# Performance work log

Hardware: AMD Instinct MI355X
Metric: run time of the kernel (lower is better)

## Reference

```python
import jax, jax.numpy as jnp
import numpy as np

HEAD_SIZE = 64
N_EMBD = 1024
B, T = 8, 4096

def setup_inputs() -> dict:
    key = jax.random.key(0)
    k1, k2, k3, k4 = jax.random.split(key, 4)
    x = jax.random.normal(k1, (B, T, N_EMBD), dtype=jnp.float32)
    # bias-free Linear weights, stored as [in, out] so y = x @ W
    scale = 1.0 / np.sqrt(N_EMBD)
    Wk = jax.random.uniform(k2, (N_EMBD, HEAD_SIZE), jnp.float32, -scale, scale)
    Wq = jax.random.uniform(k3, (N_EMBD, HEAD_SIZE), jnp.float32, -scale, scale)
    Wv = jax.random.uniform(k4, (N_EMBD, HEAD_SIZE), jnp.float32, -scale, scale)
    return {"x": x, "Wk": Wk, "Wq": Wq, "Wv": Wv}

def reference(x, Wk, Wq, Wv):
    # x: [B, T, C]
    k = x @ Wk  # [B, T, H]
    q = x @ Wq
    v = x @ Wv
    scale = HEAD_SIZE ** -0.5
    wei = jnp.einsum('bth,bsh->bts', q, k) * scale  # [B, T, T]
    Tn = x.shape[1]
    causal = jnp.tril(jnp.ones((Tn, Tn), dtype=bool))
    wei = jnp.where(causal, wei, -jnp.inf)
    wei = jax.nn.softmax(wei, axis=-1)
    # dropout p=0.0 -> identity (eval behavior)
    out = jnp.einsum('bts,bsh->bth', wei, v)  # [B, T, H]
    return out
```

## Files before the change

kernel.cpp:

```cpp
#include <hip/hip_runtime.h>
#include <hip/hip_bf16.h>


#define HS 64
#define NE 1024
#define NB 8
#define TS 4096
#define NROW (NB * TS)

#define QKV_BUF 20480
#define QKV_XB  12288

typedef __attribute__((ext_vector_type(4)))  float f32x4;
typedef __attribute__((ext_vector_type(16))) float f32x16;
typedef __attribute__((ext_vector_type(8)))  short s16x8;
typedef __attribute__((ext_vector_type(4)))  float vfloat4;

__device__ __forceinline__ unsigned short f2bf(float x) {
  return __builtin_bit_cast(unsigned short, __float2bfloat16(x));
}
__device__ __forceinline__ unsigned pkbf(float lo, float hi) {
  return (unsigned)f2bf(lo) | ((unsigned)f2bf(hi) << 16);
}

union ABFrag { s16x8 v; unsigned d[4]; };

__device__ __forceinline__ void gl_lds16(const void* g, const unsigned char* l) {
  __builtin_amdgcn_global_load_lds(
      (const __attribute__((address_space(1))) unsigned int*)(g),
      (__attribute__((address_space(3))) unsigned int*)(l), 16, 0, 0);
}

__global__ __launch_bounds__(256) void wt_kernel(const float* __restrict__ Wk,
                                                 const float* __restrict__ Wq,
                                                 const float* __restrict__ Wv,
                                                 unsigned short* __restrict__ wT2) {
  int gid = blockIdx.x * 256 + threadIdx.x;
  int j = gid & 7;
  int t1 = gid >> 3;
  int sk = t1 % 768;
  int c  = t1 / 768;
  int g = sk / 192, n = sk % 192;
  int k = c * 32 + g * 8 + j;
  const float* W = (n < 64) ? Wq : (n < 128) ? Wk : Wv;
  float s = (n < 64) ? 0.18033688011112042f : 1.0f;
  wT2[gid] = f2bf(W[k * 64 + (n & 63)] * s);
}

__global__ __launch_bounds__(256, 4) void qkv_kernel(const float* __restrict__ x,
                                                     const unsigned short* __restrict__ wT2,
                                                     unsigned short* __restrict__ q_ws,
                                                     unsigned short* __restrict__ kf,
                                                     unsigned short* __restrict__ vf) {
  __shared__ __align__(16) unsigned char smem[2 * QKV_BUF];
  const int t = threadIdx.x;
  const int w = t >> 6, lane = t & 63;
  const int g = lane >> 4, nn = lane & 15;
  const int m0blk = blockIdx.x * 64;
  const int m0 = m0blk + w * 16;

  f32x4 acc[12];
#pragma unroll
  for (int i = 0; i < 12; ++i) acc[i] = f32x4{0.f, 0.f, 0.f, 0.f};

  const unsigned short* wsrcA = wT2 + (size_t)(w * 192 + lane) * 8;
  const int wd0 = w * 3072;
  const float* xs0 = x + (size_t)(m0blk + w * 16 + 0 + (lane >> 3)) * NE + (lane & 7) * 4;
  const float* xs1 = x + (size_t)(m0blk + w * 16 + 8 + (lane >> 3)) * NE + (lane & 7) * 4;
  const int xd0 = QKV_XB + w * 2048;
  const int xd1 = xd0 + 1024;

  const int abase = QKV_XB + (w * 16 + nn) * 128 + g * 32;
  const int wbase = (g * 192 + nn) * 16;

#define ISSUE(C)                                                               \
  {                                                                            \
    unsigned char* db_ = smem + ((C) & 1) * QKV_BUF;                           \
    gl_lds16(wsrcA + (size_t)(C) * 6144, db_ + wd0);                           \
    gl_lds16(wsrcA + (size_t)(C) * 6144 + 512, db_ + wd0 + 1024);              \
    gl_lds16(wsrcA + (size_t)(C) * 6144 + 1024, db_ + wd0 + 2048);             \
    gl_lds16(xs0 + (C) * 32, db_ + xd0);                                       \
    gl_lds16(xs1 + (C) * 32, db_ + xd1);                                       \
  }

  ISSUE(0)
  __builtin_amdgcn_sched_barrier(0);
  ISSUE(1)
  __builtin_amdgcn_sched_barrier(0);

#define PHASE(C, VM, DOISS)                                                    \
  {                                                                            \
    asm volatile("s_waitcnt vmcnt(" #VM ")" ::: "memory");                     \
    __builtin_amdgcn_s_barrier();                                              \
    __builtin_amdgcn_sched_barrier(0);                                         \
    const unsigned char* bb_ = smem + ((C) & 1) * QKV_BUF;                     \
    const vfloat4 a0_ = *(const vfloat4*)(bb_ + abase);                        \
    const vfloat4 a1_ = *(const vfloat4*)(bb_ + abase + 16);                   \
    ABFrag af;                                                                 \
    af.d[0] = pkbf(a0_.x, a0_.y); af.d[1] = pkbf(a0_.z, a0_.w);                \
    af.d[2] = pkbf(a1_.x, a1_.y); af.d[3] = pkbf(a1_.z, a1_.w);                \
    _Pragma("unroll")                                                          \
    for (int i = 0; i < 12; ++i) {                                             \
      const s16x8 bf = *(const s16x8*)(bb_ + wbase + i * 256);                 \
      acc[i] = __builtin_amdgcn_mfma_f32_16x16x32_bf16(af.v, bf, acc[i], 0, 0, 0); \
    }                                                                          \
    __builtin_amdgcn_sched_barrier(0);                                         \
    __builtin_amdgcn_s_barrier();                                              \
    __builtin_amdgcn_sched_barrier(0);                                         \
    if (DOISS) { ISSUE((C) + 2) }                                              \
    __builtin_amdgcn_sched_barrier(0);                                         \
  }

#pragma unroll
  for (int c = 0; c < 30; ++c) PHASE(c, 5, 1)
  PHASE(30, 5, 0)
  PHASE(31, 0, 0)
#undef PHASE
#undef ISSUE

  const int rbase = m0 + 4 * g;
#pragma unroll
  for (int i = 0; i < 12; ++i) {
    const int c = 16 * i + nn;
#pragma unroll
    for (int j = 0; j < 4; ++j) {
      const int rr = rbase + j;
      const unsigned short hval = f2bf(acc[i][j]);
      const int b = rr >> 12, tt = rr & 4095;
      if (c < 64) {
        q_ws[(size_t)rr * HS + c] = hval;
      } else if (c < 128) {
        const int h = c - 64;
        const size_t idx = (size_t)b * 262144 + (size_t)(tt >> 5) * 2048 +
                           (h >> 4) * 512 + ((h >> 3) & 1) * 256 +
                           (tt & 31) * 8 + (h & 7);
        kf[idx] = hval;
      } else {
        const int h = c - 128;
        const size_t idx = (size_t)b * 262144 + (size_t)(tt >> 5) * 2048 +
                           (h >> 5) * 1024 + ((tt >> 4) & 1) * 512 +
                           ((tt >> 3) & 1) * 256 + (h & 31) * 8 + (tt & 7);
        vf[idx] = hval;
      }
    }
  }
}

#define TILE32F(DIAG, KF, VF, QF, M_RUN, L_RUN, O)                             \
  {                                                                            \
    f32x16 st_;                                                                \
    _Pragma("unroll") for (int r = 0; r < 16; ++r) st_[r] = 0.f;               \
    __builtin_amdgcn_s_setprio(1);                                             \
    st_ = __builtin_amdgcn_mfma_f32_32x32x16_bf16(KF[0], QF[0], st_, 0, 0, 0); \
    st_ = __builtin_amdgcn_mfma_f32_32x32x16_bf16(KF[1], QF[1], st_, 0, 0, 0); \
    st_ = __builtin_amdgcn_mfma_f32_32x32x16_bf16(KF[2], QF[2], st_, 0, 0, 0); \
    st_ = __builtin_amdgcn_mfma_f32_32x32x16_bf16(KF[3], QF[3], st_, 0, 0, 0); \
    __builtin_amdgcn_s_setprio(0);                                             \
    if (DIAG) {                                                                \
      _Pragma("unroll") for (int r = 0; r < 16; ++r) {                         \
        const int kvl_ = (r & 3) + 8 * (r >> 2) + hi4;                         \
        if (kvl_ > qi) st_[r] = -1e30f;                                        \
      }                                                                        \
    }                                                                          \
    float mx_ =                                                                \
      fmaxf(fmaxf(fmaxf(fmaxf(st_[0], st_[1]), fmaxf(st_[2], st_[3])),         \
                  fmaxf(fmaxf(st_[4], st_[5]), fmaxf(st_[6], st_[7]))),        \
            fmaxf(fmaxf(fmaxf(st_[8], st_[9]), fmaxf(st_[10], st_[11])),       \
                  fmaxf(fmaxf(st_[12], st_[13]), fmaxf(st_[14], st_[15]))));   \
    mx_ = fmaxf(mx_, __shfl_xor(mx_, 32, 64));                                 \
    const float mn_ = fmaxf(M_RUN, mx_);                                       \
    if (__ballot(mn_ > M_RUN)) {                                               \
      const float fs_ = __builtin_amdgcn_exp2f(M_RUN - mn_);                   \
      _Pragma("unroll") for (int r = 0; r < 16; ++r) {                         \
        O[0][r] *= fs_; O[1][r] *= fs_;                                        \
      }                                                                        \
      L_RUN *= fs_;                                                            \
      M_RUN = mn_;                                                             \
    }                                                                          \
    float p_[16];                                                              \
    _Pragma("unroll") for (int r = 0; r < 16; ++r)                             \
      p_[r] = __builtin_amdgcn_exp2f(st_[r] - M_RUN);                          \
    float sm_ = ((p_[0] + p_[1]) + (p_[2] + p_[3])) +                          \
                ((p_[4] + p_[5]) + (p_[6] + p_[7]));                           \
    sm_ += ((p_[8] + p_[9]) + (p_[10] + p_[11])) +                             \
           ((p_[12] + p_[13]) + (p_[14] + p_[15]));                            \
    sm_ += __shfl_xor(sm_, 32, 64);                                            \
    L_RUN += sm_;                                                              \
    const unsigned q01_ = pkbf(p_[0], p_[1]),   q23_ = pkbf(p_[2], p_[3]);     \
    const unsigned q45_ = pkbf(p_[4], p_[5]),   q67_ = pkbf(p_[6], p_[7]);     \
    const unsigned q89_ = pkbf(p_[8], p_[9]),   qab_ = pkbf(p_[10], p_[11]);   \
    const unsigned qcd_ = pkbf(p_[12], p_[13]), qef_ = pkbf(p_[14], p_[15]);   \
    const unsigned t01_ = (unsigned)__shfl_xor((int)q01_, 32, 64);             \
    const unsigned t23_ = (unsigned)__shfl_xor((int)q23_, 32, 64);             \
    const unsigned t45_ = (unsigned)__shfl_xor((int)q45_, 32, 64);             \
    const unsigned t67_ = (unsigned)__shfl_xor((int)q67_, 32, 64);             \
    const unsigned t89_ = (unsigned)__shfl_xor((int)q89_, 32, 64);             \
    const unsigned tab_ = (unsigned)__shfl_xor((int)qab_, 32, 64);             \
    const unsigned tcd_ = (unsigned)__shfl_xor((int)qcd_, 32, 64);             \
    const unsigned tef_ = (unsigned)__shfl_xor((int)qef_, 32, 64);             \
    ABFrag pf0_, pf1_;                                                         \
    pf0_.d[0] = hi ? t45_ : q01_;                                              \
    pf0_.d[1] = hi ? t67_ : q23_;                                              \
    pf0_.d[2] = hi ? q45_ : t01_;                                              \
    pf0_.d[3] = hi ? q67_ : t23_;                                              \
    pf1_.d[0] = hi ? tcd_ : q89_;                                              \
    pf1_.d[1] = hi ? tef_ : qab_;                                              \
    pf1_.d[2] = hi ? qcd_ : t89_;                                              \
    pf1_.d[3] = hi ? qef_ : tab_;                                              \
    __builtin_amdgcn_s_setprio(1);                                             \
    O[0] = __builtin_amdgcn_mfma_f32_32x32x16_bf16(VF[0], pf0_.v, O[0], 0,0,0);\
    O[0] = __builtin_amdgcn_mfma_f32_32x32x16_bf16(VF[1], pf1_.v, O[0], 0,0,0);\
    O[1] = __builtin_amdgcn_mfma_f32_32x32x16_bf16(VF[2], pf0_.v, O[1], 0,0,0);\
    O[1] = __builtin_amdgcn_mfma_f32_32x32x16_bf16(VF[3], pf1_.v, O[1], 0,0,0);\
    __builtin_amdgcn_s_setprio(0);                                             \
  }

#define LD4(dst, base)                                                         \
  dst[0] = *(const s16x8*)(base);                                              \
  dst[1] = *(const s16x8*)((base) + 512);                                      \
  dst[2] = *(const s16x8*)((base) + 1024);                                     \
  dst[3] = *(const s16x8*)((base) + 1536);

__global__ __launch_bounds__(256, 2) void attn_kernel(const unsigned short* __restrict__ q_ws,
                                                      const unsigned short* __restrict__ kf,
                                                      const unsigned short* __restrict__ vf,
                                                      float* __restrict__ out) {
  __shared__ float o_sm[2][4][16][68];
  __shared__ float lm_sm[2][4][32][2];

  const int wv = threadIdx.x >> 6, lane = threadIdx.x & 63;
  const int qi = lane & 31, hi = lane >> 5;
  const int hi8 = 8 * hi, hi4 = 4 * hi;

  const int bid = blockIdx.x;
  const int b = bid & 7;
  const int pr = bid >> 3;
  const int tiA = pr, tiB = 127 - pr;
  const int t0A = tiA * 32, t0B = tiB * 32;

  const unsigned short* kfb = kf + (size_t)b * 262144 + lane * 8;
  const unsigned short* vfb = vf + (size_t)b * 262144 + lane * 8;
  const unsigned short* qrA = q_ws + (size_t)(b * TS + t0A + qi) * HS + hi8;
  const unsigned short* qrB = q_ws + (size_t)(b * TS + t0B + qi) * HS + hi8;

  s16x8 qfA[4], qfB[4];
#pragma unroll
  for (int kk = 0; kk < 4; ++kk) {
    qfA[kk] = *(const s16x8*)(qrA + 16 * kk);
    qfB[kk] = *(const s16x8*)(qrB + 16 * kk);
  }

  f32x16 oA[2], oB[2];
#pragma unroll
  for (int r = 0; r < 16; ++r) { oA[0][r] = 0.f; oA[1][r] = 0.f; oB[0][r] = 0.f; oB[1][r] = 0.f; }
  float mA = -1e30f, lA = 0.f, mB = -1e30f, lB = 0.f;

  const int ntA = tiA + 1, ntB = tiB + 1;

  s16x8 kA[4], kB[4];
  LD4(kA, kfb + (size_t)((wv < ntA) ? wv : 0) * 2048)
  LD4(kB, kfb + (size_t)wv * 2048)

  for (int it = wv; it < ntB; it += 4) {
    const bool dA = it < ntA;
    const int nxt = it + 4;
    s16x8 vA[4], vB[4];
    LD4(vA, vfb + (size_t)(dA ? it : 0) * 2048)
    LD4(vB, vfb + (size_t)it * 2048)
    s16x8 kAn[4], kBn[4];
    LD4(kAn, kfb + (size_t)((nxt < ntA) ? nxt : 0) * 2048)
    LD4(kBn, kfb + (size_t)((nxt < ntB) ? nxt : 0) * 2048)

    if (dA) TILE32F(it == tiA, kA, vA, qfA, mA, lA, oA)
    TILE32F(it == tiB, kB, vB, qfB, mB, lB, oB)

#pragma unroll
    for (int kk = 0; kk < 4; ++kk) { kA[kk] = kAn[kk]; kB[kk] = kBn[kk]; }
  }

  if (lane < 32) {
    lm_sm[0][wv][lane][0] = mA; lm_sm[0][wv][lane][1] = lA;
    lm_sm[1][wv][lane][0] = mB; lm_sm[1][wv][lane][1] = lB;
  }
  const int q8 = (threadIdx.x >> 3) & 15;
  const int h0 = (threadIdx.x & 7) * 8;
  const int X  = threadIdx.x >> 7;
  const int t0X = X ? t0B : t0A;

#pragma unroll
  for (int P = 0; P < 2; ++P) {
    if ((qi >> 4) == P) {
      const int qr = qi & 15;
#pragma unroll
      for (int ht = 0; ht < 2; ++ht)
#pragma unroll
        for (int r = 0; r < 16; ++r) {
          const int h = ht * 32 + (r & 3) + 8 * (r >> 2) + hi4;
          o_sm[0][wv][qr][h] = oA[ht][r];
          o_sm[1][wv][qr][h] = oB[ht][r];
        }
    }
    __syncthreads();
    {
      const int q = 16 * P + q8;
      const float m0v = lm_sm[X][0][q][0], m1v = lm_sm[X][1][q][0];
      const float m2v = lm_sm[X][2][q][0], m3v = lm_sm[X][3][q][0];
      const float M = fmaxf(fmaxf(m0v, m1v), fmaxf(m2v, m3v));
      const float w0 = __builtin_amdgcn_exp2f(m0v - M);
      const float w1 = __builtin_amdgcn_exp2f(m1v - M);
      const float w2 = __builtin_amdgcn_exp2f(m2v - M);
      const float w3 = __builtin_amdgcn_exp2f(m3v - M);
      const float L = w0 * lm_sm[X][0][q][1] + w1 * lm_sm[X][1][q][1] +
                      w2 * lm_sm[X][2][q][1] + w3 * lm_sm[X][3][q][1];
      const float inv = 1.0f / L;
      float rv[8];
#pragma unroll
      for (int j = 0; j < 8; ++j)
        rv[j] = (w0 * o_sm[X][0][q8][h0 + j] + w1 * o_sm[X][1][q8][h0 + j] +
                 w2 * o_sm[X][2][q8][h0 + j] + w3 * o_sm[X][3][q8][h0 + j]) * inv;
      float* ob = out + ((size_t)(b * TS + t0X + q)) * HS + h0;
      *(float4*)(ob)     = float4{rv[0], rv[1], rv[2], rv[3]};
      *(float4*)(ob + 4) = float4{rv[4], rv[5], rv[6], rv[7]};
    }
    if (P == 0) __syncthreads();
  }
}

extern "C" void kernel_launch(void* const* d_in, const int* in_sizes, int n_in,
                              void* d_out, int out_size, void* d_ws, size_t ws_size,
                              hipStream_t stream) {
  const float* x  = (const float*)d_in[0];
  const float* Wk = (const float*)d_in[1];
  const float* Wq = (const float*)d_in[2];
  const float* Wv = (const float*)d_in[3];
  float* out = (float*)d_out;

  unsigned short* wT2  = (unsigned short*)d_ws;
  unsigned short* q_ws = wT2 + 192 * 1024;
  unsigned short* kf   = q_ws + (size_t)NROW * HS;
  unsigned short* vf   = kf + (size_t)NROW * HS;

  wt_kernel<<<dim3(768), dim3(256), 0, stream>>>(Wk, Wq, Wv, wT2);
  qkv_kernel<<<dim3(NROW / 64), dim3(256), 0, stream>>>(x, wT2, q_ws, kf, vf);
  attn_kernel<<<dim3(512), dim3(256), 0, stream>>>(q_ws, kf, vf, out);
}
```

Measured before the change: 70.98 us.

## Pair batches per block at the same query tile and drop K prefetch

Each block previously handled two mirrored query tiles (ti and 127-ti) of one batch, which gave every block equal work. It now handles the same query tile for two batches (b and b+4), scheduled from the longest causal tile down. The loop is simpler: the per-iteration branch on whether tile A is active is gone and both tiles share the diagonal test. The register double-buffering of K for the next iteration is also removed, so K and V loads are no longer overlapped with compute. Blocks now carry unequal work, which can leave the heaviest blocks setting the tail, and load latency is exposed in exchange for lower register pressure.

```diff
diff --git a/kernel.cpp b/kernel.cpp
--- a/kernel.cpp
+++ b/kernel.cpp
@@ -233,15 +233,17 @@
   const int hi8 = 8 * hi, hi4 = 4 * hi;
 
   const int bid = blockIdx.x;
-  const int b = bid & 7;
-  const int pr = bid >> 3;
-  const int tiA = pr, tiB = 127 - pr;
-  const int t0A = tiA * 32, t0B = tiB * 32;
-
-  const unsigned short* kfb = kf + (size_t)b * 262144 + lane * 8;
-  const unsigned short* vfb = vf + (size_t)b * 262144 + lane * 8;
-  const unsigned short* qrA = q_ws + (size_t)(b * TS + t0A + qi) * HS + hi8;
-  const unsigned short* qrB = q_ws + (size_t)(b * TS + t0B + qi) * HS + hi8;
+  const int ti = 127 - (bid >> 2);
+  const int bA = bid & 3, bB = bA + 4;
+  const int t0 = ti * 32;
+  const int nt = ti + 1;
+
+  const unsigned short* kfA = kf + (size_t)bA * 262144 + lane * 8;
+  const unsigned short* vfA = vf + (size_t)bA * 262144 + lane * 8;
+  const unsigned short* kfB = kf + (size_t)bB * 262144 + lane * 8;
+  const unsigned short* vfB = vf + (size_t)bB * 262144 + lane * 8;
+  const unsigned short* qrA = q_ws + (size_t)(bA * TS + t0 + qi) * HS + hi8;
+  const unsigned short* qrB = q_ws + (size_t)(bB * TS + t0 + qi) * HS + hi8;
 
   s16x8 qfA[4], qfB[4];
 #pragma unroll
@@ -255,27 +257,15 @@
   for (int r = 0; r < 16; ++r) { oA[0][r] = 0.f; oA[1][r] = 0.f; oB[0][r] = 0.f; oB[1][r] = 0.f; }
   float mA = -1e30f, lA = 0.f, mB = -1e30f, lB = 0.f;
 
-  const int ntA = tiA + 1, ntB = tiB + 1;
-
-  s16x8 kA[4], kB[4];
-  LD4(kA, kfb + (size_t)((wv < ntA) ? wv : 0) * 2048)
-  LD4(kB, kfb + (size_t)wv * 2048)
-
-  for (int it = wv; it < ntB; it += 4) {
-    const bool dA = it < ntA;
-    const int nxt = it + 4;
-    s16x8 vA[4], vB[4];
-    LD4(vA, vfb + (size_t)(dA ? it : 0) * 2048)
-    LD4(vB, vfb + (size_t)it * 2048)
-    s16x8 kAn[4], kBn[4];
-    LD4(kAn, kfb + (size_t)((nxt < ntA) ? nxt : 0) * 2048)
-    LD4(kBn, kfb + (size_t)((nxt < ntB) ? nxt : 0) * 2048)
-
-    if (dA) TILE32F(it == tiA, kA, vA, qfA, mA, lA, oA)
-    TILE32F(it == tiB, kB, vB, qfB, mB, lB, oB)
-
-#pragma unroll
-    for (int kk = 0; kk < 4; ++kk) { kA[kk] = kAn[kk]; kB[kk] = kBn[kk]; }
+  for (int it = wv; it < nt; it += 4) {
+    const bool dg = (it == ti);
+    s16x8 kA[4], kB[4], vA[4], vB[4];
+    LD4(kA, kfA + (size_t)it * 2048)
+    LD4(kB, kfB + (size_t)it * 2048)
+    LD4(vA, vfA + (size_t)it * 2048)
+    LD4(vB, vfB + (size_t)it * 2048)
+    TILE32F(dg, kA, vA, qfA, mA, lA, oA)
+    TILE32F(dg, kB, vB, qfB, mB, lB, oB)
   }
 
   if (lane < 32) {
@@ -285,7 +275,7 @@
   const int q8 = (threadIdx.x >> 3) & 15;
   const int h0 = (threadIdx.x & 7) * 8;
   const int X  = threadIdx.x >> 7;
-  const int t0X = X ? t0B : t0A;
+  const int bX = X ? bB : bA;
 
 #pragma unroll
   for (int P = 0; P < 2; ++P) {
@@ -318,7 +308,7 @@
       for (int j = 0; j < 8; ++j)
         rv[j] = (w0 * o_sm[X][0][q8][h0 + j] + w1 * o_sm[X][1][q8][h0 + j] +
                  w2 * o_sm[X][2][q8][h0 + j] + w3 * o_sm[X][3][q8][h0 + j]) * inv;
-      float* ob = out + ((size_t)(b * TS + t0X + q)) * HS + h0;
+      float* ob = out + ((size_t)(bX * TS + t0 + q)) * HS + h0;
       *(float4*)(ob)     = float4{rv[0], rv[1], rv[2], rv[3]};
       *(float4*)(ob + 4) = float4{rv[4], rv[5], rv[6], rv[7]};
     }
```

Result: slower. 78.63 us (+10.8%).

## Split paired query tiles across separate waves with 512-thread attention blocks

Applied to the files above, without the earlier changes.

Each block used 4 waves, and every wave handled both the light and the heavy causal tile. Now it launches 8 waves: waves 0-3 take one tile and waves 4-7 take the paired tile. This halves per-wave register state (one Q/O set instead of two) and lets occupancy rise to 4 blocks of 512 threads. The explicit software prefetch of the next K tile is dropped, and the waves on the light tile finish early and sit idle, so load balance inside a block gets worse.

```diff
diff --git a/kernel.cpp b/kernel.cpp
--- a/kernel.cpp
+++ b/kernel.cpp
@@ -221,7 +221,7 @@
   dst[2] = *(const s16x8*)((base) + 1024);                                     \
   dst[3] = *(const s16x8*)((base) + 1536);
 
-__global__ __launch_bounds__(256, 2) void attn_kernel(const unsigned short* __restrict__ q_ws,
+__global__ __launch_bounds__(512, 4) void attn_kernel(const unsigned short* __restrict__ q_ws,
                                                       const unsigned short* __restrict__ kf,
                                                       const unsigned short* __restrict__ vf,
                                                       float* __restrict__ out) {
@@ -235,74 +235,57 @@
   const int bid = blockIdx.x;
   const int b = bid & 7;
   const int pr = bid >> 3;
-  const int tiA = pr, tiB = 127 - pr;
-  const int t0A = tiA * 32, t0B = tiB * 32;
+  const int tile = wv >> 2;
+  const int wq = wv & 3;
+  const int ti_x = tile ? (127 - pr) : pr;
+  const int t0 = ti_x * 32;
+  const int nt = ti_x + 1;
 
   const unsigned short* kfb = kf + (size_t)b * 262144 + lane * 8;
   const unsigned short* vfb = vf + (size_t)b * 262144 + lane * 8;
-  const unsigned short* qrA = q_ws + (size_t)(b * TS + t0A + qi) * HS + hi8;
-  const unsigned short* qrB = q_ws + (size_t)(b * TS + t0B + qi) * HS + hi8;
-
-  s16x8 qfA[4], qfB[4];
-#pragma unroll
-  for (int kk = 0; kk < 4; ++kk) {
-    qfA[kk] = *(const s16x8*)(qrA + 16 * kk);
-    qfB[kk] = *(const s16x8*)(qrB + 16 * kk);
-  }
-
-  f32x16 oA[2], oB[2];
-#pragma unroll
-  for (int r = 0; r < 16; ++r) { oA[0][r] = 0.f; oA[1][r] = 0.f; oB[0][r] = 0.f; oB[1][r] = 0.f; }
-  float mA = -1e30f, lA = 0.f, mB = -1e30f, lB = 0.f;
-
-  const int ntA = tiA + 1, ntB = tiB + 1;
-
-  s16x8 kA[4], kB[4];
-  LD4(kA, kfb + (size_t)((wv < ntA) ? wv : 0) * 2048)
-  LD4(kB, kfb + (size_t)wv * 2048)
-
-  for (int it = wv; it < ntB; it += 4) {
-    const bool dA = it < ntA;
-    const int nxt = it + 4;
-    s16x8 vA[4], vB[4];
-    LD4(vA, vfb + (size_t)(dA ? it : 0) * 2048)
-    LD4(vB, vfb + (size_t)it * 2048)
-    s16x8 kAn[4], kBn[4];
-    LD4(kAn, kfb + (size_t)((nxt < ntA) ? nxt : 0) * 2048)
-    LD4(kBn, kfb + (size_t)((nxt < ntB) ? nxt : 0) * 2048)
-
-    if (dA) TILE32F(it == tiA, kA, vA, qfA, mA, lA, oA)
-    TILE32F(it == tiB, kB, vB, qfB, mB, lB, oB)
-
-#pragma unroll
-    for (int kk = 0; kk < 4; ++kk) { kA[kk] = kAn[kk]; kB[kk] = kBn[kk]; }
+  const unsigned short* qr = q_ws + (size_t)(b * TS + t0 + qi) * HS + hi8;
+
+  s16x8 qf[4];
+#pragma unroll
+  for (int kk = 0; kk < 4; ++kk) qf[kk] = *(const s16x8*)(qr + 16 * kk);
+
+  f32x16 o[2];
+#pragma unroll
+  for (int r = 0; r < 16; ++r) { o[0][r] = 0.f; o[1][r] = 0.f; }
+  float m_run = -1e30f, l_run = 0.f;
+
+  for (int it = wq; it < nt; it += 4) {
+    s16x8 kfr[4], vfr[4];
+    LD4(kfr, kfb + (size_t)it * 2048)
+    LD4(vfr, vfb + (size_t)it * 2048)
+    TILE32F(it == ti_x, kfr, vfr, qf, m_run, l_run, o)
   }
 
   if (lane < 32) {
-    lm_sm[0][wv][lane][0] = mA; lm_sm[0][wv][lane][1] = lA;
-    lm_sm[1][wv][lane][0] = mB; lm_sm[1][wv][lane][1] = lB;
-  }
-  const int q8 = (threadIdx.x >> 3) & 15;
-  const int h0 = (threadIdx.x & 7) * 8;
-  const int X  = threadIdx.x >> 7;
-  const int t0X = X ? t0B : t0A;
+    lm_sm[tile][wq][lane][0] = m_run;
+    lm_sm[tile][wq][lane][1] = l_run;
+  }
+  const int X = threadIdx.x >> 8;
+  const int rem = threadIdx.x & 255;
+  const int q8m = rem >> 4;
+  const int h0 = (rem & 15) * 4;
+  const int t0X = (X ? (127 - pr) : pr) * 32;
 
 #pragma unroll
   for (int P = 0; P < 2; ++P) {
     if ((qi >> 4) == P) {
-      const int qr = qi & 15;
+      const int qr_ = qi & 15;
 #pragma unroll
       for (int ht = 0; ht < 2; ++ht)
 #pragma unroll
         for (int r = 0; r < 16; ++r) {
           const int h = ht * 32 + (r & 3) + 8 * (r >> 2) + hi4;
-          o_sm[0][wv][qr][h] = oA[ht][r];
-          o_sm[1][wv][qr][h] = oB[ht][r];
+          o_sm[tile][wq][qr_][h] = o[ht][r];
         }
     }
     __syncthreads();
     {
-      const int q = 16 * P + q8;
+      const int q = 16 * P + q8m;
       const float m0v = lm_sm[X][0][q][0], m1v = lm_sm[X][1][q][0];
       const float m2v = lm_sm[X][2][q][0], m3v = lm_sm[X][3][q][0];
       const float M = fmaxf(fmaxf(m0v, m1v), fmaxf(m2v, m3v));
@@ -313,14 +296,13 @@
       const float L = w0 * lm_sm[X][0][q][1] + w1 * lm_sm[X][1][q][1] +
                       w2 * lm_sm[X][2][q][1] + w3 * lm_sm[X][3][q][1];
       const float inv = 1.0f / L;
-      float rv[8];
-#pragma unroll
-      for (int j = 0; j < 8; ++j)
-        rv[j] = (w0 * o_sm[X][0][q8][h0 + j] + w1 * o_sm[X][1][q8][h0 + j] +
-                 w2 * o_sm[X][2][q8][h0 + j] + w3 * o_sm[X][3][q8][h0 + j]) * inv;
-      float* ob = out + ((size_t)(b * TS + t0X + q)) * HS + h0;
-      *(float4*)(ob)     = float4{rv[0], rv[1], rv[2], rv[3]};
-      *(float4*)(ob + 4) = float4{rv[4], rv[5], rv[6], rv[7]};
+      float rv[4];
+#pragma unroll
+      for (int j = 0; j < 4; ++j)
+        rv[j] = (w0 * o_sm[X][0][q8m][h0 + j] + w1 * o_sm[X][1][q8m][h0 + j] +
+                 w2 * o_sm[X][2][q8m][h0 + j] + w3 * o_sm[X][3][q8m][h0 + j]) * inv;
+      *(float4*)(out + ((size_t)(b * TS + t0X + q)) * HS + h0) =
+          float4{rv[0], rv[1], rv[2], rv[3]};
     }
     if (P == 0) __syncthreads();
   }
@@ -342,5 +324,5 @@
 
   wt_kernel<<<dim3(768), dim3(256), 0, stream>>>(Wk, Wq, Wv, wT2);
   qkv_kernel<<<dim3(NROW / 64), dim3(256), 0, stream>>>(x, wT2, q_ws, kf, vf);
-  attn_kernel<<<dim3(512), dim3(256), 0, stream>>>(q_ws, kf, vf, out);
-}
+  attn_kernel<<<dim3(512), dim3(512), 0, stream>>>(q_ws, kf, vf, out);
+}
```

New measurement: 66.71 us. -6.0%, faster.
